# Kernel tuning notes

Hardware: AMD Instinct MI355X
Metric: run time of the kernel (lower is better)

The kernel has to match this reference:

```python
import jax, jax.numpy as jnp
import numpy as np

B, S, D, H = 2, 2048, 1024, 16
HD = D // H  # head_dim = 64


def setup_inputs() -> dict:
    key = jax.random.key(0)
    ks = jax.random.split(key, 8)
    scale = 0.02
    return {
        "hidden_states": jax.random.normal(ks[0], (B, S, D), dtype=jnp.float32),
        "attn_mask": jnp.zeros((B, 1, 1, S), dtype=jnp.float32),  # additive mask
        "Wq": jax.random.normal(ks[1], (D, D), dtype=jnp.float32) * scale,
        "bq": jnp.zeros((D,), dtype=jnp.float32),
        "Wk": jax.random.normal(ks[2], (D, D), dtype=jnp.float32) * scale,
        "bk": jnp.zeros((D,), dtype=jnp.float32),
        "Wv": jax.random.normal(ks[3], (D, D), dtype=jnp.float32) * scale,
        "bv": jnp.zeros((D,), dtype=jnp.float32),
    }


def reference(hidden_states, attn_mask, Wq, bq, Wk, bk, Wv, bv):
    # QKV projections: nn.Linear(dim, dim) -> x @ W.T + b
    def proj(x, W, b):
        y = jnp.einsum("bsd,ed->bse", x, W) + b
        # split heads: [B, S, D] -> [B, H, S, HD]
        return y.reshape(B, S, H, HD).transpose(0, 2, 1, 3)

    q = proj(hidden_states, Wq, bq)
    k = proj(hidden_states, Wk, bk)
    v = proj(hidden_states, Wv, bv)

    # scaled dot-product scores + additive mask (hack_torch_trace(scores, mask))
    scores = jnp.einsum("bhqd,bhkd->bhqk", q, k) / jnp.sqrt(jnp.float32(HD))
    scores = scores + attn_mask  # broadcast [B,1,1,S]
    probs = jax.nn.softmax(scores, axis=-1)  # attn dropout = identity (eval)

    ctx = jnp.einsum("bhqk,bhkd->bhqd", probs, v)
    # merge heads: [B, H, S, HD] -> [B, S, D]
    attn_outputs = ctx.transpose(0, 2, 1, 3).reshape(B, S, D)
    return attn_outputs
```

## Files before the change

kernel.cpp:

```cpp
#include <hip/hip_runtime.h>
#include <hip/hip_bf16.h>
#include <math.h>


typedef __bf16 bf16_t;
typedef __attribute__((ext_vector_type(8))) __bf16 bf16x8;
typedef __attribute__((ext_vector_type(4))) __bf16 bf16x4;
typedef __attribute__((ext_vector_type(4))) float f32x4;

#define B_  2
#define S_  2048
#define D_  1024
#define H_  16
#define HD_ 64
#define M_  (B_ * S_)
#define K_  D_
#define NT_ (S_ / 64)
#define LOG2E 1.44269504f
#define CS_Q (0.125f * LOG2E)

#if __has_builtin(__builtin_amdgcn_exp2f)
#define EXP2F(x) __builtin_amdgcn_exp2f(x)
#else
#define EXP2F(x) exp2f(x)
#endif

__device__ __forceinline__ f32x4 mfma16x16x32(bf16x8 a, bf16x8 b, f32x4 c) {
    return __builtin_amdgcn_mfma_f32_16x16x32_bf16(a, b, c, 0, 0, 0);
}

__device__ __forceinline__ void gload_lds16(const bf16_t* g, bf16_t* l) {
    __builtin_amdgcn_global_load_lds(
        (const __attribute__((address_space(1))) void*)g,
        (__attribute__((address_space(3))) void*)l,
        16, 0, 0);
}

__global__ void cvt_all(const float* __restrict__ hs, const float* __restrict__ wq,
                        const float* __restrict__ wk, const float* __restrict__ wv,
                        const float* __restrict__ mask,
                        bf16_t* __restrict__ Xb, bf16_t* __restrict__ Wb3,
                        float* __restrict__ wfp, bf16_t* __restrict__ wfb) {
    const int i = blockIdx.x * blockDim.x + threadIdx.x;
    if (i >= 1835008) {
        const int off = i - 1835008;
        if (off < 1024) {
            float4 v = ((const float4*)mask)[off];
            float4 w4;
            w4.x = exp2f(v.x * LOG2E); w4.y = exp2f(v.y * LOG2E);
            w4.z = exp2f(v.z * LOG2E); w4.w = exp2f(v.w * LOG2E);
            ((float4*)wfp)[off] = w4;
            const int k4 = off * 4;
            const int bb = k4 >> 11, k = k4 & 2047;
            const int t  = k >> 6,  kt = k & 63;
            const int nb = kt >> 4, kgf = (kt >> 2) & 3;
            bf16x4 wb4;
            wb4[0] = (bf16_t)w4.x; wb4[1] = (bf16_t)w4.y;
            wb4[2] = (bf16_t)w4.z; wb4[3] = (bf16_t)w4.w;
            *(bf16x4*)&wfb[(((size_t)bb * 32 + t) * 4 + kgf) * 16 + nb * 4] = wb4;
        }
        return;
    }
    const float* src; bf16_t* dst; int off;
    if (i < 1048576)      { src = hs; dst = Xb;            off = i; }
    else if (i < 1310720) { src = wq; dst = Wb3;           off = i - 1048576; }
    else if (i < 1572864) { src = wk; dst = Wb3 + 1048576; off = i - 1310720; }
    else                  { src = wv; dst = Wb3 + 2097152; off = i - 1572864; }
    float4 v = ((const float4*)src)[off];
    bf16x4 o;
    o[0] = (bf16_t)v.x; o[1] = (bf16_t)v.y;
    o[2] = (bf16_t)v.z; o[3] = (bf16_t)v.w;
    ((bf16x4*)dst)[off] = o;
}

__global__ __launch_bounds__(256, 4)
void gemm_qkv(const bf16_t* __restrict__ Xb, const bf16_t* __restrict__ Wb3,
              const float* __restrict__ bq, const float* __restrict__ bk,
              const float* __restrict__ bv,
              const float* __restrict__ wfp,
              bf16_t* __restrict__ Qo, bf16_t* __restrict__ Ko,
              bf16_t* __restrict__ Vf) {
    __shared__ bf16_t smem[2][8192];
    const int z = blockIdx.z;
    const bf16_t* Wb = Wb3 + (size_t)z * (D_ * K_);
    const float* bias = (z == 0) ? bq : (z == 1) ? bk : bv;

    const int tid  = threadIdx.x;
    const int lane = tid & 63;
    const int w    = tid >> 6;
    const int wr   = w >> 1, wc = w & 1;
    const int m0   = blockIdx.y * 128;
    const int n0   = blockIdx.x * 128;

    f32x4 acc[4][4];
    const f32x4 fzero = {0.f, 0.f, 0.f, 0.f};
#pragma unroll
    for (int i = 0; i < 4; i++)
#pragma unroll
        for (int j = 0; j < 4; j++) acc[i][j] = fzero;

    const int koff = (lane >> 4) * 8;

    auto stage = [&](int k0, int buf) {
#pragma unroll
        for (int i = 0; i < 4; i++) {
            const int chunk  = w * 4 + i;
            const int byteoff = chunk * 1024 + lane * 16;
            bf16_t* ldst = &smem[buf][chunk * 512];
            const bf16_t* gsrc;
            if (byteoff < 8192) {
                int row = byteoff >> 6;
                int col = (byteoff & 63) >> 1;
                gsrc = Xb + (size_t)(m0 + row) * K_ + k0 + col;
            } else {
                int bo  = byteoff - 8192;
                int row = bo >> 6;
                int col = (bo & 63) >> 1;
                gsrc = Wb + (size_t)(n0 + row) * K_ + k0 + col;
            }
            gload_lds16(gsrc, ldst);
        }
    };

    stage(0, 0);
    __syncthreads();

    for (int kk = 0; kk < K_ / 32; ++kk) {
        const int cur = kk & 1;
        if (kk + 1 < K_ / 32) stage((kk + 1) * 32, cur ^ 1);

        bf16x8 af[4], bfr[4];
#pragma unroll
        for (int m = 0; m < 4; m++) {
            int row = wr * 64 + m * 16 + (lane & 15);
            af[m] = *(const bf16x8*)&smem[cur][row * 32 + koff];
        }
#pragma unroll
        for (int n = 0; n < 4; n++) {
            int row = wc * 64 + n * 16 + (lane & 15);
            bfr[n] = *(const bf16x8*)&smem[cur][4096 + row * 32 + koff];
        }
#pragma unroll
        for (int m = 0; m < 4; m++)
#pragma unroll
            for (int n = 0; n < 4; n++)
                acc[m][n] = mfma16x16x32(af[m], bfr[n], acc[m][n]);

        __syncthreads();
    }

#pragma unroll
    for (int m = 0; m < 4; m++) {
        const int gm    = m0 + wr * 64 + m * 16 + ((lane >> 4) << 2);
        const int bidx  = gm >> 11;
        const int sbase = gm & 2047;
#pragma unroll
        for (int n = 0; n < 4; n++) {
            const int gn = n0 + wc * 64 + n * 16 + (lane & 15);
            const int h  = gn >> 6, hd = gn & 63;
            const float bias_v = bias[gn];
            const size_t bh = (size_t)bidx * H_ + h;
            if (z == 2) {
                const int t   = sbase >> 6, k0i = sbase & 63;
                const int nb  = k0i >> 4, kgf = (k0i >> 2) & 3;
                const int db  = hd >> 4,  lqf = hd & 15;
                const float4 w4 = *(const float4*)&wfp[bidx * S_ + sbase];
                bf16x4 pack;
                pack[0] = (bf16_t)((acc[m][n][0] + bias_v) * w4.x);
                pack[1] = (bf16_t)((acc[m][n][1] + bias_v) * w4.y);
                pack[2] = (bf16_t)((acc[m][n][2] + bias_v) * w4.z);
                pack[3] = (bf16_t)((acc[m][n][3] + bias_v) * w4.w);
                bf16_t* dst = Vf + ((bh * 32 + t) * 4 + db) * 1024 +
                    (kgf * 16 + lqf) * 16 + nb * 4;
                *(bf16x4*)dst = pack;
            } else if (z == 0) {
#pragma unroll
                for (int j = 0; j < 4; j++) {
                    float y = (acc[m][n][j] + bias_v) * CS_Q;
                    Qo[(bh * S_ + sbase + j) * HD_ + hd] = (bf16_t)y;
                }
            } else {
#pragma unroll
                for (int j = 0; j < 4; j++) {
                    float y = acc[m][n][j] + bias_v;
                    Ko[(bh * S_ + sbase + j) * HD_ + hd] = (bf16_t)y;
                }
            }
        }
    }
}

__global__ __launch_bounds__(256, 2)
void attn_fwd(const bf16_t* __restrict__ Qb, const bf16_t* __restrict__ Kb,
              const bf16_t* __restrict__ Vf, const bf16_t* __restrict__ Wfb,
              float* __restrict__ out) {
    const int flat = blockIdx.x;
    const int xcd  = flat & 7;
    const int idx  = flat >> 3;
    const int bh   = xcd * 4 + (idx >> 4);
    const int qt   = idx & 15;
    const int b    = bh >> 4;
    const int h    = bh & 15;

    const int tid  = threadIdx.x, lane = tid & 63, w = tid >> 6;

    const bf16_t* Qh = Qb + (size_t)bh * S_ * HD_;
    const bf16_t* Kh = Kb + (size_t)bh * S_ * HD_;
    const bf16_t* Vh = Vf + (size_t)bh * 32 * 4096;
    const bf16_t* Wh = Wfb + (size_t)b * 32 * 64;

    __shared__ char ShBuf[16384];

    const int lq   = lane & 15;
    const int kg   = lane >> 4;
    const int koff = kg * 8;
    const int rsub = lane >> 3;
    const int csl8 = (lane & 7) * 8;

    auto stageK = [&](int kv0, int buf) {
        bf16_t* base = (bf16_t*)(ShBuf + buf * 8192);
#pragma unroll
        for (int i = 0; i < 2; i++) {
            const int c = w * 2 + i;
            bf16_t* ldst = base + c * 512;
            const int cel = csl8 ^ (rsub * 8);
            const bf16_t* gsrc = Kh + (size_t)(kv0 + c * 8 + rsub) * HD_ + cel;
            gload_lds16(gsrc, ldst);
        }
    };

    const int qbase = qt * 128 + w * 32;
    bf16x8 qf0[2], qf1[2];
#pragma unroll
    for (int s = 0; s < 2; s++) {
        const bf16_t* qr = Qh + (size_t)(qbase + s * 16 + lq) * HD_;
        qf0[s] = *(const bf16x8*)(qr + koff);
        qf1[s] = *(const bf16x8*)(qr + 32 + koff);
    }

    const f32x4 fzero = {0.f, 0.f, 0.f, 0.f};
    f32x4 of[2][4];
    f32x4 of_l[2];
#pragma unroll
    for (int s = 0; s < 2; s++) {
        of_l[s] = fzero;
#pragma unroll
        for (int i = 0; i < 4; i++) of[s][i] = fzero;
    }

    const int rdsw = (lq & 7) << 4;

    bf16x8 vA[4], vB[4], vC[4], wA0, wA1, wB0, wB1, wC0, wC1;
    {
        const bf16_t* Vt_ = Vh;
#pragma unroll
        for (int db = 0; db < 4; db++) {
            const bf16_t* vp = Vt_ + db * 1024 + lane * 16;
            vB[db] = *(const bf16x8*)(vp);
            vC[db] = *(const bf16x8*)(vp + 8);
        }
        wB0 = *(const bf16x8*)(Wh + kg * 16);
        wB1 = *(const bf16x8*)(Wh + kg * 16 + 8);
    }
    bf16x8 vLoA[4], vHiA[4], vLoB[4], vHiB[4], vLoC[4], vHiC[4];
#pragma unroll
    for (int db = 0; db < 4; db++) { vLoB[db] = vB[db]; vHiB[db] = vC[db]; }
    stageK(0, 0);
    __syncthreads();

    f32x4 sc[2][4];

    for (int t = 0; t < NT_; ++t) {
        const int cur = t & 1;
        const char* KB = ShBuf + cur * 8192;

        bf16x8 kf0[4], kf1[4];
#pragma unroll
        for (int nb = 0; nb < 4; nb++) {
            const char* kr = KB + (nb * 16 + lq) * 128;
            kf0[nb] = *(const bf16x8*)(kr + ((kg * 16) ^ rdsw));
            kf1[nb] = *(const bf16x8*)(kr + ((64 + kg * 16) ^ rdsw));
        }

        if (t > 0) {
            bf16x8 pa0[2], pa1[2];
#pragma unroll
            for (int s = 0; s < 2; s++)
#pragma unroll
                for (int nb = 0; nb < 4; nb++)
#pragma unroll
                    for (int j = 0; j < 4; j++) {
                        float p = EXP2F(sc[s][nb][j]);
                        const int e = (nb & 1) * 4 + j;
                        if (nb < 2) pa0[s][e] = (bf16_t)p;
                        else        pa1[s][e] = (bf16_t)p;
                    }
#pragma unroll
            for (int s = 0; s < 2; s++) {
#pragma unroll
                for (int db = 0; db < 4; db++) {
                    of[s][db] = mfma16x16x32(pa0[s], vLoA[db], of[s][db]);
                    of[s][db] = mfma16x16x32(pa1[s], vHiA[db], of[s][db]);
                }
                of_l[s] = mfma16x16x32(pa0[s], wA0, of_l[s]);
                of_l[s] = mfma16x16x32(pa1[s], wA1, of_l[s]);
            }
        }

#pragma unroll
        for (int s = 0; s < 2; s++)
#pragma unroll
            for (int nb = 0; nb < 4; nb++) {
                f32x4 tacc = fzero;
                tacc = mfma16x16x32(kf0[nb], qf0[s], tacc);
                tacc = mfma16x16x32(kf1[nb], qf1[s], tacc);
                sc[s][nb] = tacc;
            }

        if (t + 1 < NT_) {
            const bf16_t* Vn = Vh + (size_t)(t + 1) * 4096;
#pragma unroll
            for (int db = 0; db < 4; db++) {
                const bf16_t* vp = Vn + db * 1024 + lane * 16;
                vLoC[db] = *(const bf16x8*)(vp);
                vHiC[db] = *(const bf16x8*)(vp + 8);
            }
            const bf16_t* wp = Wh + (size_t)(t + 1) * 64 + kg * 16;
            wC0 = *(const bf16x8*)(wp);
            wC1 = *(const bf16x8*)(wp + 8);
            stageK((t + 1) * 64, cur ^ 1);
        }

        __syncthreads();

#pragma unroll
        for (int db = 0; db < 4; db++) {
            vLoA[db] = vLoB[db]; vHiA[db] = vHiB[db];
            vLoB[db] = vLoC[db]; vHiB[db] = vHiC[db];
        }
        wA0 = wB0; wA1 = wB1;
        wB0 = wC0; wB1 = wC1;
    }

    {
        bf16x8 pa0[2], pa1[2];
#pragma unroll
        for (int s = 0; s < 2; s++)
#pragma unroll
            for (int nb = 0; nb < 4; nb++)
#pragma unroll
                for (int j = 0; j < 4; j++) {
                    float p = EXP2F(sc[s][nb][j]);
                    const int e = (nb & 1) * 4 + j;
                    if (nb < 2) pa0[s][e] = (bf16_t)p;
                    else        pa1[s][e] = (bf16_t)p;
                }
#pragma unroll
        for (int s = 0; s < 2; s++) {
#pragma unroll
            for (int db = 0; db < 4; db++) {
                of[s][db] = mfma16x16x32(pa0[s], vLoA[db], of[s][db]);
                of[s][db] = mfma16x16x32(pa1[s], vHiA[db], of[s][db]);
            }
            of_l[s] = mfma16x16x32(pa0[s], wA0, of_l[s]);
            of_l[s] = mfma16x16x32(pa1[s], wA1, of_l[s]);
        }
    }

#pragma unroll
    for (int s = 0; s < 2; s++) {
        float inv[4];
#pragma unroll
        for (int j = 0; j < 4; j++) inv[j] = 1.0f / of_l[s][j];
#pragma unroll
        for (int db = 0; db < 4; db++) {
            const int d = h * HD_ + db * 16 + lq;
#pragma unroll
            for (int j = 0; j < 4; j++) {
                const int row = qbase + s * 16 + kg * 4 + j;
                out[((size_t)b * S_ + row) * D_ + d] = of[s][db][j] * inv[j];
            }
        }
    }
}

extern "C" void kernel_launch(void* const* d_in, const int* in_sizes, int n_in,
                              void* d_out, int out_size, void* d_ws, size_t ws_size,
                              hipStream_t stream) {
    const float* hs   = (const float*)d_in[0];
    const float* mask = (const float*)d_in[1];
    const float* Wq   = (const float*)d_in[2];
    const float* bq   = (const float*)d_in[3];
    const float* Wk   = (const float*)d_in[4];
    const float* bk   = (const float*)d_in[5];
    const float* Wv   = (const float*)d_in[6];
    const float* bv   = (const float*)d_in[7];
    float* out = (float*)d_out;

    char* ws = (char*)d_ws;
    bf16_t* Xb  = (bf16_t*)(ws);
    bf16_t* Wb3 = (bf16_t*)(ws + 8388608);
    bf16_t* Qb  = (bf16_t*)(ws + 14680064);
    bf16_t* Kb  = (bf16_t*)(ws + 23068672);
    bf16_t* Vfr = (bf16_t*)(ws + 31457280);
    float*  wfp = (float*)(ws + 39845888);
    bf16_t* wfb = (bf16_t*)(ws + 39862272);

    cvt_all<<<7172, 256, 0, stream>>>(hs, Wq, Wk, Wv, mask, Xb, Wb3, wfp, wfb);

    dim3 ggrid(D_ / 128, M_ / 128, 3);
    gemm_qkv<<<ggrid, 256, 0, stream>>>(Xb, Wb3, bq, bk, bv, wfp, Qb, Kb, Vfr);

    attn_fwd<<<512, 256, 0, stream>>>(Qb, Kb, Vfr, wfb, out);
}
```

Baseline: 86.49 us.

## Stage V tiles through LDS alongside K with async global-to-LDS loads

Instead of each wave loading V fragments straight from global memory into registers two tiles ahead, V is now staged into double-buffered LDS together with K, using the same direct global-to-LDS loads, and then read from LDS. The aim is to cut per-wave redundant global/L2 traffic and register pressure from the triple-buffered V registers. The cost is doubled LDS per block, which may lower occupancy, plus extra LDS reads each iteration. The W vector is still loaded from global, now issued in the same iteration it is used.

```diff
diff --git a/kernel.cpp b/kernel.cpp
--- a/kernel.cpp
+++ b/kernel.cpp
@@ -209,7 +209,7 @@
     const bf16_t* Vh = Vf + (size_t)bh * 32 * 4096;
     const bf16_t* Wh = Wfb + (size_t)b * 32 * 64;
 
-    __shared__ char ShBuf[16384];
+    __shared__ char ShBuf[32768];
 
     const int lq   = lane & 15;
     const int kg   = lane >> 4;
@@ -217,14 +217,23 @@
     const int rsub = lane >> 3;
     const int csl8 = (lane & 7) * 8;
 
-    auto stageK = [&](int kv0, int buf) {
-        bf16_t* base = (bf16_t*)(ShBuf + buf * 8192);
-#pragma unroll
-        for (int i = 0; i < 2; i++) {
-            const int c = w * 2 + i;
+    auto stageKV = [&](int t, int buf) {
+        bf16_t* base = (bf16_t*)(ShBuf + buf * 16384);
+        const int kv0 = t * 64;
+        const bf16_t* Vt_ = Vh + (size_t)t * 4096;
+#pragma unroll
+        for (int i = 0; i < 4; i++) {
+            const int c = w * 4 + i;
             bf16_t* ldst = base + c * 512;
-            const int cel = csl8 ^ (rsub * 8);
-            const bf16_t* gsrc = Kh + (size_t)(kv0 + c * 8 + rsub) * HD_ + cel;
+            const bf16_t* gsrc;
+            if (c < 8) {
+                const int cel = csl8 ^ (rsub * 8);
+                gsrc = Kh + (size_t)(kv0 + c * 8 + rsub) * HD_ + cel;
+            } else if (c < 12) {
+                gsrc = Vt_ + (c - 8) * 1024 + lane * 16;
+            } else {
+                gsrc = Vt_ + (c - 12) * 1024 + lane * 16 + 8;
+            }
             gload_lds16(gsrc, ldst);
         }
     };
@@ -250,29 +259,16 @@
 
     const int rdsw = (lq & 7) << 4;
 
-    bf16x8 vA[4], vB[4], vC[4], wA0, wA1, wB0, wB1, wC0, wC1;
-    {
-        const bf16_t* Vt_ = Vh;
-#pragma unroll
-        for (int db = 0; db < 4; db++) {
-            const bf16_t* vp = Vt_ + db * 1024 + lane * 16;
-            vB[db] = *(const bf16x8*)(vp);
-            vC[db] = *(const bf16x8*)(vp + 8);
-        }
-        wB0 = *(const bf16x8*)(Wh + kg * 16);
-        wB1 = *(const bf16x8*)(Wh + kg * 16 + 8);
-    }
-    bf16x8 vLoA[4], vHiA[4], vLoB[4], vHiB[4], vLoC[4], vHiC[4];
-#pragma unroll
-    for (int db = 0; db < 4; db++) { vLoB[db] = vB[db]; vHiB[db] = vC[db]; }
-    stageK(0, 0);
+    bf16x8 vLoC[4], vHiC[4], vLoN[4], vHiN[4], wC0, wC1, wN0, wN1;
+
+    stageKV(0, 0);
     __syncthreads();
 
     f32x4 sc[2][4];
 
     for (int t = 0; t < NT_; ++t) {
         const int cur = t & 1;
-        const char* KB = ShBuf + cur * 8192;
+        const char* KB = ShBuf + cur * 16384;
 
         bf16x8 kf0[4], kf1[4];
 #pragma unroll
@@ -280,6 +276,18 @@
             const char* kr = KB + (nb * 16 + lq) * 128;
             kf0[nb] = *(const bf16x8*)(kr + ((kg * 16) ^ rdsw));
             kf1[nb] = *(const bf16x8*)(kr + ((64 + kg * 16) ^ rdsw));
+        }
+
+#pragma unroll
+        for (int db = 0; db < 4; db++) {
+            const char* vlo = KB + 8192 + db * 1024 + lane * 16;
+            vLoN[db] = *(const bf16x8*)(vlo);
+            vHiN[db] = *(const bf16x8*)(vlo + 4096);
+        }
+        {
+            const bf16_t* wp = Wh + (size_t)t * 64 + kg * 16;
+            wN0 = *(const bf16x8*)(wp);
+            wN1 = *(const bf16x8*)(wp + 8);
         }
 
         if (t > 0) {
@@ -299,11 +307,11 @@
             for (int s = 0; s < 2; s++) {
 #pragma unroll
                 for (int db = 0; db < 4; db++) {
-                    of[s][db] = mfma16x16x32(pa0[s], vLoA[db], of[s][db]);
-                    of[s][db] = mfma16x16x32(pa1[s], vHiA[db], of[s][db]);
+                    of[s][db] = mfma16x16x32(pa0[s], vLoC[db], of[s][db]);
+                    of[s][db] = mfma16x16x32(pa1[s], vHiC[db], of[s][db]);
                 }
-                of_l[s] = mfma16x16x32(pa0[s], wA0, of_l[s]);
-                of_l[s] = mfma16x16x32(pa1[s], wA1, of_l[s]);
+                of_l[s] = mfma16x16x32(pa0[s], wC0, of_l[s]);
+                of_l[s] = mfma16x16x32(pa1[s], wC1, of_l[s]);
             }
         }
 
@@ -317,29 +325,15 @@
                 sc[s][nb] = tacc;
             }
 
-        if (t + 1 < NT_) {
-            const bf16_t* Vn = Vh + (size_t)(t + 1) * 4096;
-#pragma unroll
-            for (int db = 0; db < 4; db++) {
-                const bf16_t* vp = Vn + db * 1024 + lane * 16;
-                vLoC[db] = *(const bf16x8*)(vp);
-                vHiC[db] = *(const bf16x8*)(vp + 8);
-            }
-            const bf16_t* wp = Wh + (size_t)(t + 1) * 64 + kg * 16;
-            wC0 = *(const bf16x8*)(wp);
-            wC1 = *(const bf16x8*)(wp + 8);
-            stageK((t + 1) * 64, cur ^ 1);
-        }
+        if (t + 1 < NT_) stageKV(t + 1, cur ^ 1);
 
         __syncthreads();
 
 #pragma unroll
         for (int db = 0; db < 4; db++) {
-            vLoA[db] = vLoB[db]; vHiA[db] = vHiB[db];
-            vLoB[db] = vLoC[db]; vHiB[db] = vHiC[db];
-        }
-        wA0 = wB0; wA1 = wB1;
-        wB0 = wC0; wB1 = wC1;
+            vLoC[db] = vLoN[db]; vHiC[db] = vHiN[db];
+        }
+        wC0 = wN0; wC1 = wN1;
     }
 
     {
@@ -359,11 +353,11 @@
         for (int s = 0; s < 2; s++) {
 #pragma unroll
             for (int db = 0; db < 4; db++) {
-                of[s][db] = mfma16x16x32(pa0[s], vLoA[db], of[s][db]);
-                of[s][db] = mfma16x16x32(pa1[s], vHiA[db], of[s][db]);
-            }
-            of_l[s] = mfma16x16x32(pa0[s], wA0, of_l[s]);
-            of_l[s] = mfma16x16x32(pa1[s], wA1, of_l[s]);
+                of[s][db] = mfma16x16x32(pa0[s], vLoC[db], of[s][db]);
+                of[s][db] = mfma16x16x32(pa1[s], vHiC[db], of[s][db]);
+            }
+            of_l[s] = mfma16x16x32(pa0[s], wC0, of_l[s]);
+            of_l[s] = mfma16x16x32(pa1[s], wC1, of_l[s]);
         }
     }
 
```

New measurement: 88.27 us. 2.1% more time.
